# Optimization experiments

Measured on AMD Instinct MI355X. Metric: run time of the kernel, lower is better.

## Reference

```python
import jax, jax.numpy as jnp
import numpy as np

HID = 256
NL = 4
NC = 5
SPACE = 16


def _grid_sample(feat, grid):
    # feat [B,C,H,W]; grid [B,Hg,Wg,2] in [-1,1]; bilinear, align_corners=True, zeros padding
    B, C, H, W = feat.shape
    x = (grid[..., 0] + 1.0) * 0.5 * (W - 1)
    y = (grid[..., 1] + 1.0) * 0.5 * (H - 1)
    x0f = jnp.floor(x)
    y0f = jnp.floor(y)
    wx1 = x - x0f
    wy1 = y - y0f

    def corner(yf, xf, wgt):
        valid = (xf >= 0) & (xf <= W - 1) & (yf >= 0) & (yf <= H - 1)
        xi = jnp.clip(xf, 0, W - 1).astype(jnp.int32)
        yi = jnp.clip(yf, 0, H - 1).astype(jnp.int32)
        v = jax.vmap(lambda f, yy, xx: f[:, yy, xx])(feat, yi, xi)  # [B,C,Hg,Wg]
        return v * (wgt * valid.astype(feat.dtype))[:, None]

    return (corner(y0f, x0f, (1 - wy1) * (1 - wx1))
            + corner(y0f, x0f + 1, (1 - wy1) * wx1)
            + corner(y0f + 1, x0f, wy1 * (1 - wx1))
            + corner(y0f + 1, x0f + 1, wy1 * wx1))


def _conv(x, w, b, pad):
    y = jax.lax.conv_general_dilated(x, w, (1, 1), ((pad, pad), (pad, pad)),
                                     dimension_numbers=('NCHW', 'OIHW', 'NCHW'))
    return y + b[None, :, None, None]


def _resize_ac(x, oh, ow):
    # bilinear resize with align_corners=True
    B, C, H, W = x.shape
    ys = jnp.linspace(0.0, H - 1.0, oh)
    xs = jnp.linspace(0.0, W - 1.0, ow)
    y0 = jnp.floor(ys).astype(jnp.int32)
    y1 = jnp.minimum(y0 + 1, H - 1)
    x0 = jnp.floor(xs).astype(jnp.int32)
    x1 = jnp.minimum(x0 + 1, W - 1)
    wy = (ys - y0)[None, None, :, None]
    wx = (xs - x0)[None, None, None, :]
    top = x[:, :, y0, :] * (1 - wy) + x[:, :, y1, :] * wy
    return top[:, :, :, x0] * (1 - wx) + top[:, :, :, x1] * wx


def _mlp(x, w1, b1, w2, b2):
    # 2-layer MLP, dropout is identity at inference
    return jax.nn.relu(x @ w1 + b1) @ w2 + b2


def setup_inputs() -> dict:
    key = jax.random.key(0)
    ks = jax.random.split(key, 16)
    B, H, W = 8, 512, 512

    def rn(k, shape, s=0.02):
        return jax.random.normal(k, shape, jnp.float32) * s

    return {
        'images': jax.random.normal(ks[0], (B, 3, H, W), jnp.float32),
        'feat0': jax.random.normal(ks[1], (B, HID, 128, 128), jnp.float32),
        'feat1': jax.random.normal(ks[2], (B, HID, 64, 64), jnp.float32),
        'feat2': jax.random.normal(ks[3], (B, HID, 32, 32), jnp.float32),
        'feat3': jax.random.normal(ks[4], (B, HID, 16, 16), jnp.float32),
        'mask_feat': jax.random.normal(ks[5], (B, HID, 128, 128), jnp.float32),
        'o': jax.random.normal(ks[6], (B, 16, 16, 768), jnp.float32),
        'dw1': rn(ks[7], (768, HID)), 'db1': jnp.zeros((HID,), jnp.float32),
        'dw2': rn(ks[8], (HID, 8)), 'db2': jnp.zeros((8,), jnp.float32),
        'cw1': rn(ks[9], (HID, HID)), 'cb1': jnp.zeros((HID,), jnp.float32),
        'cw2': rn(ks[10], (HID, NC + 1)), 'cb2': jnp.zeros((NC + 1,), jnp.float32),
        'conv_w': rn(ks[11], (HID, HID * NL, 3, 3)), 'conv_b': jnp.zeros((HID,), jnp.float32),
        'mw1': rn(ks[12], (HID, HID, 3, 3)), 'mb1': jnp.zeros((HID,), jnp.float32),
        'bn_g': jnp.ones((HID,), jnp.float32), 'bn_b': jnp.zeros((HID,), jnp.float32),
        'bn_m': jnp.zeros((HID,), jnp.float32), 'bn_v': jnp.ones((HID,), jnp.float32),
        'mw2': rn(ks[13], (1, HID, 1, 1)), 'mb2': jnp.zeros((1,), jnp.float32),
    }


def reference(images, feat0, feat1, feat2, feat3, mask_feat, o,
              dw1, db1, dw2, db2, cw1, cb1, cw2, cb2, conv_w, conv_b,
              mw1, mb1, bn_g, bn_b, bn_m, bn_v, mw2, mb2):
    B, _, H, W = images.shape
    ny = int(np.ceil(H / SPACE))
    nx = int(np.ceil(W / SPACE))
    # AnchorPoints: meshgrid 'xy', scaled by space, shifted by half-cell origin
    gx, gy = jnp.meshgrid(jnp.arange(nx, dtype=jnp.float32), jnp.arange(ny, dtype=jnp.float32))
    origin = jnp.array([(W % SPACE) or SPACE, (H % SPACE) or SPACE], jnp.float32) / 2
    anchors = jnp.stack([gx, gy], -1) * SPACE + origin  # [ny,nx,2] (x,y)

    # learned offsets: MLP then pixel-shuffle style 16x16x8 -> 32x32x2
    d = _mlp(o, dw1, db1, dw2, db2)  # [B,16,16,8]
    d = d.reshape(B, 16, 16, 2, 2, 2).transpose(0, 1, 3, 2, 4, 5).reshape(B, 32, 32, 2)
    prop = anchors[None] + d  # deformed proposals [B,32,32,2]

    feats = [feat0, feat1, feat2, feat3]
    strides = [4, 8, 16, 32]
    rois = []
    for f, s in zip(feats, strides):
        fh, fw = f.shape[2], f.shape[3]
        grid = 2.0 * prop / s / jnp.array([fw, fh], jnp.float32) - 1.0
        rois.append(_grid_sample(f, grid))
    roi = jnp.concatenate(rois, 1)  # [B, HID*NL, 32, 32]
    roi = _conv(roi, conv_w, conv_b, 1).transpose(0, 2, 3, 1)  # [B,32,32,HID]
    logits = _mlp(roi, cw1, cb1, cw2, cb2)  # [B,32,32,NC+1]

    # mask head: conv3x3 -> BN(eval) -> ReLU -> conv1x1(pad=1) -> bilinear upsample (align_corners=True)
    m = _conv(mask_feat, mw1, mb1, 1)
    m = m * (bn_g * jax.lax.rsqrt(bn_v + 1e-5))[None, :, None, None] \
        + (bn_b - bn_m * bn_g * jax.lax.rsqrt(bn_v + 1e-5))[None, :, None, None]
    m = jax.nn.relu(m)
    m = _conv(m, mw2, mb2, 1)  # 1x1 conv with padding=1 -> [B,1,130,130] (as in source)
    masks = _resize_ac(m, H, W)  # [B,1,H,W]

    return (prop.reshape(B, -1, 2), logits.reshape(B, -1, NC + 1), masks)
```

## Files before the change

### kernel.cpp

```cpp
#include <hip/hip_runtime.h>
#include <hip/hip_bf16.h>
#include <cstdint>
#include <cstddef>

using bf16x8 = __attribute__((ext_vector_type(8))) short;
using f32x4  = __attribute__((ext_vector_type(4))) float;

static constexpr size_t PART_OFF = 4194308;
static constexpr size_t WT_OFF   = 16777220;
static constexpr size_t WTR_SH   = (size_t)294912 * 8;
static constexpr size_t WTM_SH   = (size_t)73728 * 8;
static constexpr size_t M2P_OFF  = WT_OFF + (WTR_SH + WTM_SH) / 2;

__device__ __forceinline__ uint32_t pk2(float a, float b) {
  __hip_bfloat162 h = __float22bfloat162_rn(make_float2(a, b));
  union { __hip_bfloat162 h; uint32_t u; } c; c.h = h;
  return c.u;
}

__device__ __forceinline__ void gld16(const void* g, void* l) {
  __builtin_amdgcn_global_load_lds(
      (const __attribute__((address_space(1))) void*)g,
      (__attribute__((address_space(3))) void*)l, 16, 0, 0);
}

#define CBAR(N) do { \
    asm volatile("s_waitcnt vmcnt(" #N ")" ::: "memory"); \
    __builtin_amdgcn_sched_barrier(0); \
    __builtin_amdgcn_s_barrier(); \
    __builtin_amdgcn_sched_barrier(0); } while (0)

__global__ __launch_bounds__(256) void k_prep_w(
    const float* __restrict__ conv_w, const float* __restrict__ mw1,
    short* __restrict__ wTr, short* __restrict__ wTm, float* __restrict__ zp) {
  __shared__ float sm[16 * 292];
  int t = threadIdx.x;
  int bid = blockIdx.x;
  if (bid == 0 && t < 4) zp[t] = 0.f;
  bool is_m = (bid >= 512);
  int b2 = is_m ? (bid - 512) : bid;
  int kidx = is_m ? (b2 & 7) : (b2 & 31);
  int cog  = is_m ? (b2 >> 3) : (b2 >> 5);
  const float* src = is_m ? mw1 : conv_w;
  short* dst = is_m ? wTm : wTr;
  int CI = is_m ? 256 : 1024;
  int ci0 = kidx * 32;
  int co0 = cog * 16;
  for (int e = t; e < 4608; e += 256) {
    int row = e / 288, pos = e - row * 288;
    sm[row * 292 + pos] = src[((size_t)(co0 + row) * CI + ci0) * 9 + pos];
  }
  __syncthreads();
  int nb = cog >> 3, cofrag = cog & 7;
  for (int e = t; e < 576; e += 256) {
    int tap = e >> 6, kg = (e >> 4) & 3, lr = e & 15;
    float v[8];
#pragma unroll
    for (int j = 0; j < 8; ++j) v[j] = sm[lr * 292 + (kg * 8 + j) * 9 + tap];
    uint4 pk = make_uint4(pk2(v[0], v[1]), pk2(v[2], v[3]),
                          pk2(v[4], v[5]), pk2(v[6], v[7]));
    size_t chunk = ((size_t)(kidx * 2 + nb) * 9 + tap) * 512
                 + cofrag * 64 + kg * 16 + lr;
    *(uint4*)&dst[chunk * 8] = pk;
  }
}

__global__ __launch_bounds__(256) void k_prop(
    const float* __restrict__ o,
    const float* __restrict__ dw1, const float* __restrict__ db1,
    const float* __restrict__ dw2, const float* __restrict__ db2,
    float* __restrict__ prop) {
  __shared__ float o_lds[4 * 768];
  __shared__ float h_lds[4 * 256];
  int t = threadIdx.x;
  int bid = blockIdx.x;
  int b = bid >> 6;
  int rem = bid & 63;
  int i = rem >> 2;
  int j0 = (rem & 3) * 4;
  const float* obase = o + ((size_t)(b * 16 + i) * 16 + j0) * 768;
  for (int e = t; e < 4 * 768; e += 256) o_lds[e] = obase[e];
  __syncthreads();
  float h0 = 0.f, h1 = 0.f, h2 = 0.f, h3 = 0.f;
  for (int k = 0; k < 768; ++k) {
    float w = dw1[k * 256 + t];
    h0 = fmaf(o_lds[k], w, h0);
    h1 = fmaf(o_lds[768 + k], w, h1);
    h2 = fmaf(o_lds[1536 + k], w, h2);
    h3 = fmaf(o_lds[2304 + k], w, h3);
  }
  float bb = db1[t];
  h_lds[t]        = fmaxf(h0 + bb, 0.f);
  h_lds[256 + t]  = fmaxf(h1 + bb, 0.f);
  h_lds[512 + t]  = fmaxf(h2 + bb, 0.f);
  h_lds[768 + t]  = fmaxf(h3 + bb, 0.f);
  __syncthreads();
  if (t < 32) {
    int pos = t >> 3;
    int c   = t & 7;
    float acc = db2[c];
    const float* hp = h_lds + pos * 256;
    for (int k = 0; k < 256; ++k) acc = fmaf(hp[k], dw2[k * 8 + c], acc);
    int p = c >> 2, q = (c >> 1) & 1, cc = c & 1;
    int row = 2 * i + p;
    int col = 2 * (j0 + pos) + q;
    float anchor = (cc == 0) ? ((float)col * 16.f + 8.f) : ((float)row * 16.f + 8.f);
    prop[((size_t)(b * 32 + row) * 32 + col) * 2 + cc] = anchor + acc;
  }
}

__global__ __launch_bounds__(256) void k_sample(
    const float* __restrict__ f0, const float* __restrict__ f1,
    const float* __restrict__ f2, const float* __restrict__ f3,
    const float* __restrict__ prop, uint4* __restrict__ bfR) {
  int py = blockIdx.x;
  int l  = blockIdx.y;
  int b  = blockIdx.z;
  int t  = threadIdx.x;
  int xq = t & 31;
  int cq = t >> 5;
  const float* f = (l == 0) ? f0 : (l == 1) ? f1 : (l == 2) ? f2 : f3;
  int fsz = 128 >> l;
  float s = (float)(4 << l);

  size_t pidx = ((size_t)b * 32 + py) * 32 + xq;
  float px = prop[pidx * 2 + 0];
  float pv = prop[pidx * 2 + 1];
  float gx = 2.f * px / s / (float)fsz - 1.f;
  float gy = 2.f * pv / s / (float)fsz - 1.f;
  float x = (gx + 1.f) * 0.5f * (float)(fsz - 1);
  float y = (gy + 1.f) * 0.5f * (float)(fsz - 1);
  float x0f = floorf(x), y0f = floorf(y);
  float wx1 = x - x0f, wy1 = y - y0f;

  int off[4];
  float wgt[4];
#pragma unroll
  for (int cy = 0; cy < 2; ++cy) {
#pragma unroll
    for (int cx = 0; cx < 2; ++cx) {
      float xf = x0f + (float)cx;
      float yf = y0f + (float)cy;
      float w = (cy ? wy1 : (1.f - wy1)) * (cx ? wx1 : (1.f - wx1));
      bool valid = (xf >= 0.f) && (xf <= (float)(fsz - 1)) &&
                   (yf >= 0.f) && (yf <= (float)(fsz - 1));
      int xi = (int)fminf(fmaxf(xf, 0.f), (float)(fsz - 1));
      int yi = (int)fminf(fmaxf(yf, 0.f), (float)(fsz - 1));
      off[cy * 2 + cx] = yi * fsz + xi;
      wgt[cy * 2 + cx] = valid ? w : 0.f;
    }
  }
  const float* fb = f + (size_t)b * 256 * fsz * fsz;
#pragma unroll
  for (int i = 0; i < 4; ++i) {
    int cgl = i * 8 + cq;
    float v[8];
#pragma unroll
    for (int j = 0; j < 8; ++j) {
      const float* fc = fb + (size_t)(cgl * 8 + j) * fsz * fsz;
      v[j] = wgt[0] * fc[off[0]] + wgt[1] * fc[off[1]] +
             wgt[2] * fc[off[2]] + wgt[3] * fc[off[3]];
    }
    bfR[(((size_t)b * 128 + l * 32 + cgl) * 32 + py) * 32 + xq] =
        make_uint4(pk2(v[0], v[1]), pk2(v[2], v[3]),
                   pk2(v[4], v[5]), pk2(v[6], v[7]));
  }
}

__global__ __launch_bounds__(256) void k_cvt(const float* __restrict__ mf,
                                             uint4* __restrict__ bfA) {
  int d = blockIdx.x * 256 + threadIdx.x;
  int x = d & 127, y = (d >> 7) & 127, cg = (d >> 14) & 31, b = d >> 19;
  const float* src = mf + (((size_t)(b * 256 + cg * 8)) << 14) + (y << 7) + x;
  float v[8];
#pragma unroll
  for (int j = 0; j < 8; ++j) v[j] = src[(size_t)j << 14];
  bfA[d] = make_uint4(pk2(v[0], v[1]), pk2(v[2], v[3]),
                      pk2(v[4], v[5]), pk2(v[6], v[7]));
}

__global__ __launch_bounds__(512, 2) void k_roi_mfma(
    const uint4* __restrict__ bfR, const short* __restrict__ wTr,
    float* __restrict__ part) {
  __shared__ __align__(16) short A_s[2][1408 * 8];
  __shared__ __align__(16) short B_s[4608 * 8];
  int t = threadIdx.x;
  int lane = t & 63, wv = t >> 6, wm = wv >> 1, wn = wv & 1;
  int kg = lane >> 4, lr = lane & 15;
  int bid = blockIdx.x;
  int nb = bid & 1;
  int mi = (bid >> 1) & 31;
  int b = mi >> 2, yt = mi & 3;
  int ks = bid >> 6;

  f32x4 acc[4][4];
#pragma unroll
  for (int m = 0; m < 4; ++m)
#pragma unroll
    for (int n = 0; n < 4; ++n) acc[m][n] = {0.f, 0.f, 0.f, 0.f};

  bf16x8 Af[2][4], Bf[2][4];

  const uint4* aptr[3];
  int astep[3], aldst[3];
  bool aon[3];
#pragma unroll
  for (int i = 0; i < 3; ++i) {
    int wq = wv + 8 * i;
    aon[i] = wq < 22;
    int c = wq * 64 + lane;
    int pxi = c >> 2, slot = c & 3;
    int r = pxi / 34;
    int x = pxi - r * 34 - 1;
    int y = yt * 8 + r - 1;
    int cg4 = slot ^ ((pxi >> 1) & 3);
    bool ok = (r < 10) && (x >= 0) && (x < 32) && (y >= 0) && (y < 32);
    long chunk = ok ? (long)((((b * 128 + ks * 32 + cg4) * 32 + y) * 32) + x) : -1L;
    aptr[i] = bfR + chunk;
    astep[i] = ok ? 4096 : 0;
    aldst[i] = wq * 512;
  }
  const size_t BKC = (size_t)4608 * 8;
  const short* bbase = wTr + ((size_t)(ks * 8) * 2 + nb) * BKC;

#define ROI_ISSUE_A(BUF)                                         \
  {                                                              \
    _Pragma("unroll")                                            \
    for (int i = 0; i < 3; ++i)                                  \
      if (aon[i]) {                                              \
        gld16(aptr[i], &A_s[BUF][aldst[i]]);                     \
        aptr[i] += astep[i];                                     \
      }                                                          \
  }
#define ROI_ISSUE_H1(KC)                                         \
  {                                                              \
    const short* bk = bbase + (size_t)(KC) * 2 * BKC;            \
    _Pragma("unroll")                                            \
    for (int j = 0; j < 5; ++j) {                                \
      int w = wv + 8 * j;                                        \
      gld16(bk + (w * 64 + lane) * 8, &B_s[w * 512]);            \
    }                                                            \
  }
#define ROI_ISSUE_H2(KC)                                         \
  {                                                              \
    const short* bk = bbase + (size_t)(KC) * 2 * BKC;            \
    _Pragma("unroll")                                            \
    for (int j = 0; j < 4; ++j) {                                \
      int w = wv + 8 * j;                                        \
      gld16(bk + (2560 + w * 64 + lane) * 8,                     \
            &B_s[20480 + w * 512]);                              \
    }                                                            \
  }

#define ROI_LOADF(PB, TAP)                                                        \
  {                                                                               \
    int ky = (TAP) / 3, kx = (TAP) - ky * 3;                                      \
    _Pragma("unroll")                                                             \
    for (int n = 0; n < 4; ++n)                                                   \
      Bf[PB][n] = *(const bf16x8*)&B_s[((((TAP) * 8 + wn * 4 + n) * 4 + kg) * 16  \
                                        + lr) * 8];                               \
    _Pragma("unroll")                                                             \
    for (int m = 0; m < 4; ++m) {                                                 \
      int pb = wm * 64 + m * 16;                                                  \
      int px = ((pb >> 5) + ky) * 34 + (pb & 31) + lr + kx;                       \
      Af[PB][m] = *(const bf16x8*)&As[(px * 4 + ((kg ^ (px >> 1)) & 3)) * 8];     \
    }                                                                             \
  }
#define ROI_MMA(PB)                                                               \
  {                                                                               \
    _Pragma("unroll")                                                             \
    for (int m = 0; m < 4; ++m)                                                   \
      _Pragma("unroll")                                                           \
      for (int n = 0; n < 4; ++n)                                                 \
        acc[m][n] = __builtin_amdgcn_mfma_f32_16x16x32_bf16(Af[PB][m], Bf[PB][n], \
                                                            acc[m][n], 0, 0, 0);  \
  }
#define ROI_REGION(T0, T1)                                                        \
  {                                                                               \
    ROI_LOADF(0, T0);                                                             \
    _Pragma("unroll")                                                             \
    for (int tp = (T0); tp < (T1); ++tp) {                                        \
      if (tp + 1 < (T1)) { ROI_LOADF((tp + 1) & 1, tp + 1); }                     \
      ROI_MMA(tp & 1);                                                            \
    }                                                                             \
  }

  ROI_ISSUE_H1(0);
  ROI_ISSUE_A(0);
  __syncthreads();

  for (int kc = 0; kc < 7; ++kc) {
    int buf = kc & 1;
    const short* As = A_s[buf];
    ROI_ISSUE_H2(kc);
    ROI_ISSUE_A(buf ^ 1);
    __builtin_amdgcn_s_setprio(1);
    ROI_REGION(0, 5);
    __builtin_amdgcn_s_setprio(0);
    CBAR(2);
    ROI_ISSUE_H1(kc + 1);
    __builtin_amdgcn_s_setprio(1);
    ROI_REGION(5, 9);
    __builtin_amdgcn_s_setprio(0);
    CBAR(0);
  }
  {
    const short* As = A_s[1];
    ROI_ISSUE_H2(7);
    __builtin_amdgcn_s_setprio(1);
    ROI_REGION(0, 5);
    __builtin_amdgcn_s_setprio(0);
    CBAR(0);
    __builtin_amdgcn_s_setprio(1);
    ROI_REGION(5, 9);
    __builtin_amdgcn_s_setprio(0);
  }
#pragma unroll
  for (int m = 0; m < 4; ++m)
#pragma unroll
    for (int r = 0; r < 4; ++r) {
      int p = wm * 64 + m * 16 + kg * 4 + r;
      int y = yt * 8 + (p >> 5), x = p & 31;
      float* dst = part + (size_t)ks * 2097152 + (((size_t)b * 32 + y) * 32 + x) * 256
                        + nb * 128 + wn * 64 + lr;
#pragma unroll
      for (int n = 0; n < 4; ++n) dst[n * 16] = acc[m][n][r];
    }
}

__global__ __launch_bounds__(256) void k_mlp(
    const float* __restrict__ part, const float* __restrict__ conv_b,
    const float* __restrict__ cw1, const float* __restrict__ cb1,
    const float* __restrict__ cw2, const float* __restrict__ cb2,
    float* __restrict__ logits) {
  __shared__ float v[1024];
  __shared__ float h[1024];
  int t = threadIdx.x;
  size_t base = (size_t)blockIdx.x * 1024;
  const size_t CH = (size_t)8192 * 256;
  for (int e = t; e < 1024; e += 256) {
    float s = part[base + e] + part[CH + base + e] +
              part[2 * CH + base + e] + part[3 * CH + base + e];
    v[e] = s + conv_b[e & 255];
  }
  __syncthreads();
  float a0 = cb1[t], a1 = a0, a2 = a0, a3 = a0;
  for (int k = 0; k < 256; ++k) {
    float w = cw1[k * 256 + t];
    a0 = fmaf(v[k], w, a0);
    a1 = fmaf(v[256 + k], w, a1);
    a2 = fmaf(v[512 + k], w, a2);
    a3 = fmaf(v[768 + k], w, a3);
  }
  h[t]       = fmaxf(a0, 0.f);
  h[256 + t] = fmaxf(a1, 0.f);
  h[512 + t] = fmaxf(a2, 0.f);
  h[768 + t] = fmaxf(a3, 0.f);
  __syncthreads();
  if (t < 24) {
    int pos = t / 6, c = t - 6 * pos;
    float acc = cb2[c];
    const float* hp = h + pos * 256;
    for (int k = 0; k < 256; ++k) acc = fmaf(hp[k], cw2[k * 6 + c], acc);
    logits[((size_t)blockIdx.x * 4 + pos) * 6 + c] = acc;
  }
}

__global__ __launch_bounds__(512, 2) void k_mask_mfma(
    const uint4* __restrict__ bfA, const short* __restrict__ wTm,
    const float* __restrict__ mb1,
    const float* __restrict__ bn_g, const float* __restrict__ bn_b,
    const float* __restrict__ bn_m, const float* __restrict__ bn_v,
    const float* __restrict__ mw2, float* __restrict__ m2p) {
  __shared__ __align__(16) short A_s[2][2112 * 8];
  __shared__ __align__(16) short B_s[4608 * 8];
  int t = threadIdx.x;
  int lane = t & 63, wv = t >> 6, wm = wv >> 1, wn = wv & 1;
  int kg = lane >> 4, lr = lane & 15;
  int bid = blockIdx.x;
  int nb = bid & 1;
  int tile = bid >> 1;
  int b = tile >> 6, yt = tile & 63;

  f32x4 acc[4][4];
#pragma unroll
  for (int m = 0; m < 4; ++m)
#pragma unroll
    for (int n = 0; n < 4; ++n) acc[m][n] = {0.f, 0.f, 0.f, 0.f};

  bf16x8 Af[2][4], Bf[2][4];

  const uint4* aptr[5];
  int astep[5], aldst[5];
  bool aon[5];
#pragma unroll
  for (int i = 0; i < 5; ++i) {
    int wq = wv + 8 * i;
    aon[i] = wq < 33;
    int c = wq * 64 + lane;
    int pxi = c >> 2, slot = c & 3;
    int r = pxi / 130;
    int x = pxi - r * 130 - 1;
    int y = 2 * yt + r - 1;
    int cg4 = slot ^ ((pxi >> 1) & 3);
    bool ok = (r < 4) && (x >= 0) && (x < 128) && (y >= 0) && (y < 128);
    long chunk = ok ? (long)((((b * 32 + cg4) * 128 + y) * 128) + x) : -1L;
    aptr[i] = bfA + chunk;
    astep[i] = ok ? 65536 : 0;
    aldst[i] = wq * 512;
  }
  const size_t BKC = (size_t)4608 * 8;
  const short* bbase = wTm + (size_t)nb * BKC;

#define MSK_ISSUE_A(BUF)                                         \
  {                                                              \
    _Pragma("unroll")                                            \
    for (int i = 0; i < 5; ++i)                                  \
      if (aon[i]) {                                              \
        gld16(aptr[i], &A_s[BUF][aldst[i]]);                     \
        aptr[i] += astep[i];                                     \
      }                                                          \
  }
#define MSK_ISSUE_H1(KC)                                         \
  {                                                              \
    const short* bk = bbase + (size_t)(KC) * 2 * BKC;            \
    _Pragma("unroll")                                            \
    for (int j = 0; j < 5; ++j) {                                \
      int w = wv + 8 * j;                                        \
      gld16(bk + (w * 64 + lane) * 8, &B_s[w * 512]);            \
    }                                                            \
  }
#define MSK_ISSUE_H2(KC)                                         \
  {                                                              \
    const short* bk = bbase + (size_t)(KC) * 2 * BKC;            \
    _Pragma("unroll")                                            \
    for (int j = 0; j < 4; ++j) {                                \
      int w = wv + 8 * j;                                        \
      gld16(bk + (2560 + w * 64 + lane) * 8,                     \
            &B_s[20480 + w * 512]);                              \
    }                                                            \
  }

#define MSK_LOADF(PB, TAP)                                                        \
  {                                                                               \
    int ky = (TAP) / 3, kx = (TAP) - ky * 3;                                      \
    _Pragma("unroll")                                                             \
    for (int n = 0; n < 4; ++n)                                                   \
      Bf[PB][n] = *(const bf16x8*)&B_s[((((TAP) * 8 + wn * 4 + n) * 4 + kg) * 16  \
                                        + lr) * 8];                               \
    _Pragma("unroll")                                                             \
    for (int m = 0; m < 4; ++m) {                                                 \
      int px = ((wm >> 1) + ky) * 130 + (wm & 1) * 64 + m * 16 + lr + kx;         \
      Af[PB][m] = *(const bf16x8*)&As[(px * 4 + ((kg ^ (px >> 1)) & 3)) * 8];     \
    }                                                                             \
  }
#define MSK_MMA(PB)                                                               \
  {                                                                               \
    _Pragma("unroll")                                                             \
    for (int m = 0; m < 4; ++m)                                                   \
      _Pragma("unroll")                                                           \
      for (int n = 0; n < 4; ++n)                                                 \
        acc[m][n] = __builtin_amdgcn_mfma_f32_16x16x32_bf16(Af[PB][m], Bf[PB][n], \
                                                            acc[m][n], 0, 0, 0);  \
  }
#define MSK_REGION(T0, T1)                                                        \
  {                                                                               \
    MSK_LOADF(0, T0);                                                             \
    _Pragma("unroll")                                                             \
    for (int tp = (T0); tp < (T1); ++tp) {                                        \
      if (tp + 1 < (T1)) { MSK_LOADF((tp + 1) & 1, tp + 1); }                     \
      MSK_MMA(tp & 1);                                                            \
    }                                                                             \
  }

  MSK_ISSUE_H1(0);
  MSK_ISSUE_A(0);
  __syncthreads();

  for (int kc = 0; kc < 7; ++kc) {
    int buf = kc & 1;
    const short* As = A_s[buf];
    MSK_ISSUE_H2(kc);
    MSK_ISSUE_A(buf ^ 1);
    __builtin_amdgcn_s_setprio(1);
    MSK_REGION(0, 5);
    __builtin_amdgcn_s_setprio(0);
    CBAR(4);
    MSK_ISSUE_H1(kc + 1);
    __builtin_amdgcn_s_setprio(1);
    MSK_REGION(5, 9);
    __builtin_amdgcn_s_setprio(0);
    CBAR(0);
  }
  {
    const short* As = A_s[1];
    MSK_ISSUE_H2(7);
    __builtin_amdgcn_s_setprio(1);
    MSK_REGION(0, 5);
    __builtin_amdgcn_s_setprio(0);
    CBAR(0);
    __builtin_amdgcn_s_setprio(1);
    MSK_REGION(5, 9);
    __builtin_amdgcn_s_setprio(0);
  }

  float sc[4], sh[4], w2v[4], b1[4];
#pragma unroll
  for (int n = 0; n < 4; ++n) {
    int co = nb * 128 + wn * 64 + n * 16 + lr;
    float s = bn_g[co] * rsqrtf(bn_v[co] + 1e-5f);
    sc[n] = s;
    sh[n] = bn_b[co] - bn_m[co] * s;
    b1[n] = mb1[co];
    w2v[n] = mw2[co];
  }
  float* red = (float*)&A_s[0][0];
#pragma unroll
  for (int m = 0; m < 4; ++m)
#pragma unroll
    for (int r = 0; r < 4; ++r) {
      int p = (wm >> 1) * 128 + (wm & 1) * 64 + m * 16 + kg * 4 + r;
      float s = 0.f;
#pragma unroll
      for (int n = 0; n < 4; ++n) {
        float z = fmaf(acc[m][n][r] + b1[n], sc[n], sh[n]);
        s = fmaf(w2v[n], fmaxf(z, 0.f), s);
      }
      red[p * 32 + wn * 16 + lr] = s;
    }
  __syncthreads();
  if (t < 256) {
    float s = 0.f;
#pragma unroll
    for (int q = 0; q < 32; ++q) s += red[t * 32 + q];
    int y = 2 * yt + (t >> 7);
    int x = t & 127;
    m2p[(size_t)nb * 131072 + ((size_t)b * 128 + y) * 128 + x] = s;
  }
}

__global__ __launch_bounds__(256) void k_resize(const float* __restrict__ m2p,
                                                const float* __restrict__ mb2,
                                                float* __restrict__ masks) {
  int idx = blockIdx.x * 256 + threadIdx.x;
  int b = idx >> 18;
  int rem = idx & 262143;
  int y = rem >> 9;
  int x = rem & 511;
  const float SC = 129.0f / 511.0f;
  float sy = (float)y * SC;
  float sx = (float)x * SC;
  float y0f = floorf(sy), x0f = floorf(sx);
  int y0 = (int)y0f, x0 = (int)x0f;
  int y1 = min(y0 + 1, 129), x1 = min(x0 + 1, 129);
  float wy = sy - y0f, wx = sx - x0f;
  float base = mb2[0];
  const float* p0 = m2p + (size_t)b * 16384;
  const float* p1 = m2p + 131072 + (size_t)b * 16384;

  auto corner = [&](int yy, int xx) -> float {
    if (yy >= 1 && yy <= 128 && xx >= 1 && xx <= 128) {
      int o2 = (yy - 1) * 128 + (xx - 1);
      return base + p0[o2] + p1[o2];
    }
    return base;
  };
  float tv = corner(y0, x0) * (1.f - wx) + corner(y0, x1) * wx;
  float bv = corner(y1, x0) * (1.f - wx) + corner(y1, x1) * wx;
  masks[idx] = tv * (1.f - wy) + bv * wy;
}

extern "C" void kernel_launch(void* const* d_in, const int* in_sizes, int n_in,
                              void* d_out, int out_size, void* d_ws, size_t ws_size,
                              hipStream_t stream) {
  (void)in_sizes; (void)n_in; (void)out_size; (void)ws_size;
  const float* f0        = (const float*)d_in[1];
  const float* f1        = (const float*)d_in[2];
  const float* f2        = (const float*)d_in[3];
  const float* f3        = (const float*)d_in[4];
  const float* mask_feat = (const float*)d_in[5];
  const float* o         = (const float*)d_in[6];
  const float* dw1       = (const float*)d_in[7];
  const float* db1       = (const float*)d_in[8];
  const float* dw2       = (const float*)d_in[9];
  const float* db2       = (const float*)d_in[10];
  const float* cw1       = (const float*)d_in[11];
  const float* cb1       = (const float*)d_in[12];
  const float* cw2       = (const float*)d_in[13];
  const float* cb2       = (const float*)d_in[14];
  const float* conv_w    = (const float*)d_in[15];
  const float* conv_b    = (const float*)d_in[16];
  const float* mw1       = (const float*)d_in[17];
  const float* mb1       = (const float*)d_in[18];
  const float* bn_g      = (const float*)d_in[19];
  const float* bn_b      = (const float*)d_in[20];
  const float* bn_m      = (const float*)d_in[21];
  const float* bn_v      = (const float*)d_in[22];
  const float* mw2       = (const float*)d_in[23];
  const float* mb2       = (const float*)d_in[24];

  float* ws   = (float*)d_ws;
  uint4* bf   = (uint4*)(ws + 4);
  float* part = ws + PART_OFF;
  short* wTr  = (short*)(ws + WT_OFF);
  short* wTm  = wTr + WTR_SH;
  float* m2p  = ws + M2P_OFF;

  float* out_prop   = (float*)d_out;
  float* out_logits = out_prop + (size_t)8 * 1024 * 2;
  float* out_masks  = out_logits + (size_t)8 * 1024 * 6;

  hipLaunchKernelGGL(k_prep_w, dim3(640), dim3(256), 0, stream,
                     conv_w, mw1, wTr, wTm, ws);
  hipLaunchKernelGGL(k_prop, dim3(512), dim3(256), 0, stream,
                     o, dw1, db1, dw2, db2, out_prop);
  hipLaunchKernelGGL(k_sample, dim3(32, 4, 8), dim3(256), 0, stream,
                     f0, f1, f2, f3, out_prop, bf);
  hipLaunchKernelGGL(k_roi_mfma, dim3(256), dim3(512), 0, stream,
                     bf, wTr, part);
  hipLaunchKernelGGL(k_mlp, dim3(2048), dim3(256), 0, stream,
                     part, conv_b, cw1, cb1, cw2, cb2, out_logits);
  hipLaunchKernelGGL(k_cvt, dim3(16384), dim3(256), 0, stream,
                     mask_feat, bf);
  hipLaunchKernelGGL(k_mask_mfma, dim3(1024), dim3(512), 0, stream,
                     bf, wTm, mb1, bn_g, bn_b, bn_m, bn_v, mw2, m2p);
  hipLaunchKernelGGL(k_resize, dim3(8192), dim3(256), 0, stream,
                     m2p, mb2, out_masks);
}
```

Baseline: 336.4 us.

## Single-buffer mask conv LDS tiles so two blocks fit per CU

The mask 3x3 conv MFMA kernel drops its double-buffered A tile and its full 9-tap B tile. It now keeps one A buffer and a B buffer sized for five taps, reused for taps 0-4 and then 5-8. This shrinks the kernel's shared memory to roughly half, which should let two 512-thread blocks reside per CU as the launch bounds request. The cost is that global-to-LDS loads no longer overlap with MFMA work inside a block, since each phase waits on vmcnt(0) and a barrier. Overlap then has to come from the second resident block.

```diff
diff --git a/kernel.cpp b/kernel.cpp
--- a/kernel.cpp
+++ b/kernel.cpp
@@ -26,6 +26,11 @@
 
 #define CBAR(N) do { \
     asm volatile("s_waitcnt vmcnt(" #N ")" ::: "memory"); \
+    __builtin_amdgcn_sched_barrier(0); \
+    __builtin_amdgcn_s_barrier(); \
+    __builtin_amdgcn_sched_barrier(0); } while (0)
+
+#define BAR() do { \
     __builtin_amdgcn_sched_barrier(0); \
     __builtin_amdgcn_s_barrier(); \
     __builtin_amdgcn_sched_barrier(0); } while (0)
@@ -372,8 +377,8 @@
     const float* __restrict__ bn_g, const float* __restrict__ bn_b,
     const float* __restrict__ bn_m, const float* __restrict__ bn_v,
     const float* __restrict__ mw2, float* __restrict__ m2p) {
-  __shared__ __align__(16) short A_s[2][2112 * 8];
-  __shared__ __align__(16) short B_s[4608 * 8];
+  __shared__ __align__(16) short A_s[2080 * 8];
+  __shared__ __align__(16) short B_s[2560 * 8];
   int t = threadIdx.x;
   int lane = t & 63, wv = t >> 6, wm = wv >> 1, wn = wv & 1;
   int kg = lane >> 4, lr = lane & 15;
@@ -412,16 +417,16 @@
   const size_t BKC = (size_t)4608 * 8;
   const short* bbase = wTm + (size_t)nb * BKC;
 
-#define MSK_ISSUE_A(BUF)                                         \
+#define MSK_ISSUE_A()                                            \
   {                                                              \
     _Pragma("unroll")                                            \
     for (int i = 0; i < 5; ++i)                                  \
       if (aon[i]) {                                              \
-        gld16(aptr[i], &A_s[BUF][aldst[i]]);                     \
+        gld16(aptr[i], &A_s[aldst[i]]);                          \
         aptr[i] += astep[i];                                     \
       }                                                          \
   }
-#define MSK_ISSUE_H1(KC)                                         \
+#define MSK_ISSUE_B05(KC)                                        \
   {                                                              \
     const short* bk = bbase + (size_t)(KC) * 2 * BKC;            \
     _Pragma("unroll")                                            \
@@ -430,28 +435,27 @@
       gld16(bk + (w * 64 + lane) * 8, &B_s[w * 512]);            \
     }                                                            \
   }
-#define MSK_ISSUE_H2(KC)                                         \
+#define MSK_ISSUE_B59(KC)                                        \
   {                                                              \
     const short* bk = bbase + (size_t)(KC) * 2 * BKC;            \
     _Pragma("unroll")                                            \
     for (int j = 0; j < 4; ++j) {                                \
       int w = wv + 8 * j;                                        \
-      gld16(bk + (2560 + w * 64 + lane) * 8,                     \
-            &B_s[20480 + w * 512]);                              \
+      gld16(bk + (2560 + w * 64 + lane) * 8, &B_s[w * 512]);     \
     }                                                            \
   }
 
-#define MSK_LOADF(PB, TAP)                                                        \
+#define MSK_LOADF(PB, TAP, TAPL)                                                  \
   {                                                                               \
     int ky = (TAP) / 3, kx = (TAP) - ky * 3;                                      \
     _Pragma("unroll")                                                             \
     for (int n = 0; n < 4; ++n)                                                   \
-      Bf[PB][n] = *(const bf16x8*)&B_s[((((TAP) * 8 + wn * 4 + n) * 4 + kg) * 16  \
+      Bf[PB][n] = *(const bf16x8*)&B_s[((((TAPL) * 8 + wn * 4 + n) * 4 + kg) * 16 \
                                         + lr) * 8];                               \
     _Pragma("unroll")                                                             \
     for (int m = 0; m < 4; ++m) {                                                 \
       int px = ((wm >> 1) + ky) * 130 + (wm & 1) * 64 + m * 16 + lr + kx;         \
-      Af[PB][m] = *(const bf16x8*)&As[(px * 4 + ((kg ^ (px >> 1)) & 3)) * 8];     \
+      Af[PB][m] = *(const bf16x8*)&A_s[(px * 4 + ((kg ^ (px >> 1)) & 3)) * 8];    \
     }                                                                             \
   }
 #define MSK_MMA(PB)                                                               \
@@ -463,45 +467,30 @@
         acc[m][n] = __builtin_amdgcn_mfma_f32_16x16x32_bf16(Af[PB][m], Bf[PB][n], \
                                                             acc[m][n], 0, 0, 0);  \
   }
-#define MSK_REGION(T0, T1)                                                        \
+#define MSK_REGION(T0, T1, TL0)                                                   \
   {                                                                               \
-    MSK_LOADF(0, T0);                                                             \
+    MSK_LOADF(0, T0, (T0) - (TL0));                                               \
     _Pragma("unroll")                                                             \
     for (int tp = (T0); tp < (T1); ++tp) {                                        \
-      if (tp + 1 < (T1)) { MSK_LOADF((tp + 1) & 1, tp + 1); }                     \
+      if (tp + 1 < (T1)) { MSK_LOADF((tp + 1) & 1, tp + 1, tp + 1 - (TL0)); }     \
       MSK_MMA(tp & 1);                                                            \
     }                                                                             \
   }
 
-  MSK_ISSUE_H1(0);
-  MSK_ISSUE_A(0);
-  __syncthreads();
-
-  for (int kc = 0; kc < 7; ++kc) {
-    int buf = kc & 1;
-    const short* As = A_s[buf];
-    MSK_ISSUE_H2(kc);
-    MSK_ISSUE_A(buf ^ 1);
-    __builtin_amdgcn_s_setprio(1);
-    MSK_REGION(0, 5);
-    __builtin_amdgcn_s_setprio(0);
-    CBAR(4);
-    MSK_ISSUE_H1(kc + 1);
-    __builtin_amdgcn_s_setprio(1);
-    MSK_REGION(5, 9);
-    __builtin_amdgcn_s_setprio(0);
-    CBAR(0);
-  }
-  {
-    const short* As = A_s[1];
-    MSK_ISSUE_H2(7);
-    __builtin_amdgcn_s_setprio(1);
-    MSK_REGION(0, 5);
-    __builtin_amdgcn_s_setprio(0);
+  for (int kc = 0; kc < 8; ++kc) {
+    MSK_ISSUE_A();
+    MSK_ISSUE_B05(kc);
     CBAR(0);
     __builtin_amdgcn_s_setprio(1);
-    MSK_REGION(5, 9);
+    MSK_REGION(0, 5, 0);
     __builtin_amdgcn_s_setprio(0);
+    BAR();
+    MSK_ISSUE_B59(kc);
+    CBAR(0);
+    __builtin_amdgcn_s_setprio(1);
+    MSK_REGION(5, 9, 5);
+    __builtin_amdgcn_s_setprio(0);
+    BAR();
   }
 
   float sc[4], sh[4], w2v[4], b1[4];
@@ -514,7 +503,7 @@
     b1[n] = mb1[co];
     w2v[n] = mw2[co];
   }
-  float* red = (float*)&A_s[0][0];
+  float* red = (float*)&A_s[0];
 #pragma unroll
   for (int m = 0; m < 4; ++m)
 #pragma unroll
```

Result: slower. 357.2 us (+6.2%).

## Load mask-conv A fragments directly from global, dropping LDS staging

Applied to the files above, without the earlier changes.

The mask 3x3 conv MFMA kernel no longer stages the input activation halo tile in shared memory through double-buffered async global-to-LDS loads. Each wave now reads its A fragments straight from global memory for every tap, handling the padding borders with clamping and zero-fill. This frees about 67KB of LDS per block, which may raise occupancy and removes the A-side LDS traffic. In exchange it adds nine redundant global/L2 reads per k-chunk with exposed latency, plus an extra full barrier between tap regions because the loads are no longer pipelined.

```diff
diff --git a/kernel.cpp b/kernel.cpp
--- a/kernel.cpp
+++ b/kernel.cpp
@@ -22,6 +22,10 @@
   __builtin_amdgcn_global_load_lds(
       (const __attribute__((address_space(1))) void*)g,
       (__attribute__((address_space(3))) void*)l, 16, 0, 0);
+}
+
+__device__ __forceinline__ bf16x8 ld_bf8(const uint4* p) {
+  union { uint4 u; bf16x8 v; } c; c.u = *p; return c.v;
 }
 
 #define CBAR(N) do { \
@@ -372,7 +376,6 @@
     const float* __restrict__ bn_g, const float* __restrict__ bn_b,
     const float* __restrict__ bn_m, const float* __restrict__ bn_v,
     const float* __restrict__ mw2, float* __restrict__ m2p) {
-  __shared__ __align__(16) short A_s[2][2112 * 8];
   __shared__ __align__(16) short B_s[4608 * 8];
   int t = threadIdx.x;
   int lane = t & 63, wv = t >> 6, wm = wv >> 1, wn = wv & 1;
@@ -381,6 +384,7 @@
   int nb = bid & 1;
   int tile = bid >> 1;
   int b = tile >> 6, yt = tile & 63;
+  int wmx = wm & 1, wmr = wm >> 1;
 
   f32x4 acc[4][4];
 #pragma unroll
@@ -389,38 +393,15 @@
     for (int n = 0; n < 4; ++n) acc[m][n] = {0.f, 0.f, 0.f, 0.f};
 
   bf16x8 Af[2][4], Bf[2][4];
-
-  const uint4* aptr[5];
-  int astep[5], aldst[5];
-  bool aon[5];
-#pragma unroll
-  for (int i = 0; i < 5; ++i) {
-    int wq = wv + 8 * i;
-    aon[i] = wq < 33;
-    int c = wq * 64 + lane;
-    int pxi = c >> 2, slot = c & 3;
-    int r = pxi / 130;
-    int x = pxi - r * 130 - 1;
-    int y = 2 * yt + r - 1;
-    int cg4 = slot ^ ((pxi >> 1) & 3);
-    bool ok = (r < 4) && (x >= 0) && (x < 128) && (y >= 0) && (y < 128);
-    long chunk = ok ? (long)((((b * 32 + cg4) * 128 + y) * 128) + x) : -1L;
-    aptr[i] = bfA + chunk;
-    astep[i] = ok ? 65536 : 0;
-    aldst[i] = wq * 512;
-  }
+  const bf16x8 z8 = {0, 0, 0, 0, 0, 0, 0, 0};
+
+  const uint4* akc = bfA + ((size_t)(b * 32 + kg) << 14);
+  int yb = 2 * yt + wmr - 1;
+  int xl = wmx * 64 + lr - 1;
+
   const size_t BKC = (size_t)4608 * 8;
   const short* bbase = wTm + (size_t)nb * BKC;
 
-#define MSK_ISSUE_A(BUF)                                         \
-  {                                                              \
-    _Pragma("unroll")                                            \
-    for (int i = 0; i < 5; ++i)                                  \
-      if (aon[i]) {                                              \
-        gld16(aptr[i], &A_s[BUF][aldst[i]]);                     \
-        aptr[i] += astep[i];                                     \
-      }                                                          \
-  }
 #define MSK_ISSUE_H1(KC)                                         \
   {                                                              \
     const short* bk = bbase + (size_t)(KC) * 2 * BKC;            \
@@ -443,15 +424,26 @@
 
 #define MSK_LOADF(PB, TAP)                                                        \
   {                                                                               \
-    int ky = (TAP) / 3, kx = (TAP) - ky * 3;                                      \
+    const int ky = (TAP) / 3, kx = (TAP) - ky * 3;                                \
     _Pragma("unroll")                                                             \
     for (int n = 0; n < 4; ++n)                                                   \
       Bf[PB][n] = *(const bf16x8*)&B_s[((((TAP) * 8 + wn * 4 + n) * 4 + kg) * 16  \
                                         + lr) * 8];                               \
-    _Pragma("unroll")                                                             \
-    for (int m = 0; m < 4; ++m) {                                                 \
-      int px = ((wm >> 1) + ky) * 130 + (wm & 1) * 64 + m * 16 + lr + kx;         \
-      Af[PB][m] = *(const bf16x8*)&As[(px * 4 + ((kg ^ (px >> 1)) & 3)) * 8];     \
+    int y = yb + ky;                                                              \
+    if ((unsigned)y < 128u) {                                                     \
+      const uint4* ay = akc + y * 128;                                            \
+      _Pragma("unroll")                                                           \
+      for (int m = 0; m < 4; ++m) {                                               \
+        int x = xl + m * 16 + kx;                                                 \
+        if (m == 0 && kx == 0) x = (x < 0) ? 0 : x;                               \
+        if (m == 3 && kx == 2) x = (x > 127) ? 127 : x;                           \
+        Af[PB][m] = ld_bf8(ay + x);                                               \
+      }                                                                           \
+      if (kx == 0) { if (wmx == 0) Af[PB][0] = (lr == 0)  ? z8 : Af[PB][0]; }     \
+      if (kx == 2) { if (wmx == 1) Af[PB][3] = (lr == 15) ? z8 : Af[PB][3]; }     \
+    } else {                                                                      \
+      _Pragma("unroll")                                                           \
+      for (int m = 0; m < 4; ++m) Af[PB][m] = z8;                                 \
     }                                                                             \
   }
 #define MSK_MMA(PB)                                                               \
@@ -474,34 +466,20 @@
   }
 
   MSK_ISSUE_H1(0);
-  MSK_ISSUE_A(0);
-  __syncthreads();
-
-  for (int kc = 0; kc < 7; ++kc) {
-    int buf = kc & 1;
-    const short* As = A_s[buf];
+  CBAR(0);
+
+  for (int kc = 0; kc < 8; ++kc) {
     MSK_ISSUE_H2(kc);
-    MSK_ISSUE_A(buf ^ 1);
     __builtin_amdgcn_s_setprio(1);
     MSK_REGION(0, 5);
     __builtin_amdgcn_s_setprio(0);
-    CBAR(4);
-    MSK_ISSUE_H1(kc + 1);
+    CBAR(0);
+    if (kc < 7) MSK_ISSUE_H1(kc + 1);
     __builtin_amdgcn_s_setprio(1);
     MSK_REGION(5, 9);
     __builtin_amdgcn_s_setprio(0);
     CBAR(0);
-  }
-  {
-    const short* As = A_s[1];
-    MSK_ISSUE_H2(7);
-    __builtin_amdgcn_s_setprio(1);
-    MSK_REGION(0, 5);
-    __builtin_amdgcn_s_setprio(0);
-    CBAR(0);
-    __builtin_amdgcn_s_setprio(1);
-    MSK_REGION(5, 9);
-    __builtin_amdgcn_s_setprio(0);
+    akc += 65536;
   }
 
   float sc[4], sh[4], w2v[4], b1[4];
@@ -514,12 +492,12 @@
     b1[n] = mb1[co];
     w2v[n] = mw2[co];
   }
-  float* red = (float*)&A_s[0][0];
+  float* red = (float*)&B_s[0];
 #pragma unroll
   for (int m = 0; m < 4; ++m)
 #pragma unroll
     for (int r = 0; r < 4; ++r) {
-      int p = (wm >> 1) * 128 + (wm & 1) * 64 + m * 16 + kg * 4 + r;
+      int p = wmr * 128 + wmx * 64 + m * 16 + kg * 4 + r;
       float s = 0.f;
 #pragma unroll
       for (int n = 0; n < 4; ++n) {
```

Result: slower. 351.0 us (+4.3%).
